# Kernel tuning notes

Hardware: AMD Instinct MI355X
Metric: run time of the kernel (lower is better)

## Reference

```python
import jax, jax.numpy as jnp
import numpy as np

N = 200_000   # nodes
E = 6_400_000 # edges (avg degree 32)


def setup_inputs() -> dict:
    key = jax.random.key(0)
    k = jax.random.split(key, 6)
    x = jax.random.normal(k[0], (N, 2), dtype=jnp.float32)
    edge_index = jax.random.randint(k[1], (2, E), 0, N, dtype=jnp.int32)
    # GCNConv(2, 8) and GCNConv(8, 4) parameters (Glorot-ish init, zero bias as in PyG)
    W1 = jax.random.normal(k[2], (2, 8), dtype=jnp.float32) * (1.0 / np.sqrt(2.0))
    b1 = jnp.zeros((8,), dtype=jnp.float32)
    W2 = jax.random.normal(k[3], (8, 4), dtype=jnp.float32) * (1.0 / np.sqrt(8.0))
    b2 = jnp.zeros((4,), dtype=jnp.float32)
    return {"x": x, "edge_index": edge_index, "W1": W1, "b1": b1, "W2": W2, "b2": b2}


def _gcn_conv(x, src, dst, norm, W, b, n):
    # PyG GCNConv: linear transform, normalized gather/scatter-add, bias after aggregation
    h = x @ W                                   # [N, F_out]
    msg = h[src] * norm[:, None]                # gather + edge-wise scale, [E', F_out]
    agg = jax.ops.segment_sum(msg, dst, num_segments=n)  # scatter-add at targets
    return agg + b


def reference(x, edge_index, W1, b1, W2, b2):
    n = x.shape[0]
    # add self-loops (PyG default add_self_loops=True)
    loops = jnp.arange(n, dtype=edge_index.dtype)
    src = jnp.concatenate([edge_index[0], loops])
    dst = jnp.concatenate([edge_index[1], loops])
    # symmetric degree normalization: deg computed at targets with unit edge weights
    deg = jax.ops.segment_sum(jnp.ones_like(src, dtype=x.dtype), dst, num_segments=n)
    deg_inv_sqrt = jnp.where(deg > 0, jax.lax.rsqrt(jnp.maximum(deg, 1.0)), 0.0)
    norm = deg_inv_sqrt[src] * deg_inv_sqrt[dst]  # [E']

    h = jax.nn.relu(_gcn_conv(x, src, dst, norm, W1, b1, n))
    out = _gcn_conv(h, src, dst, norm, W2, b2, n)
    return out
```

## Files before the change

### kernel.cpp

```cpp
#include <hip/hip_runtime.h>


#define EPB   8192
#define PART  2048
#define LPBIT 11
#define SRCB  18
#define BC    4
#define RSTR  2049
#define CAP   69632
#define STCAP 17408


__global__ __launch_bounds__(512) void sortA_kernel(
    const int* __restrict__ src, const int* __restrict__ dst,
    int* __restrict__ cursor, unsigned* __restrict__ packed, int E, int P) {
    __shared__ int cnt[128];
    int tid = threadIdx.x;
    if (tid < 128) cnt[tid] = 0;
    __syncthreads();
    int nv4 = E >> 2;
    int b4 = (blockIdx.x * EPB) >> 2;
    const int4* d4 = (const int4*)dst;
    const int4* s4 = (const int4*)src;
    int4 dv[4], sv[4];
    bool inb[4];
    #pragma unroll
    for (int k = 0; k < 4; k++) {
        int i = b4 + k * 512 + tid;
        inb[k] = (i < nv4);
        if (inb[k]) {
            dv[k] = d4[i];
            sv[k] = s4[i];
            atomicAdd(&cnt[dv[k].x >> LPBIT], 1);
            atomicAdd(&cnt[dv[k].y >> LPBIT], 1);
            atomicAdd(&cnt[dv[k].z >> LPBIT], 1);
            atomicAdd(&cnt[dv[k].w >> LPBIT], 1);
        }
    }
    bool lastblk = (blockIdx.x == gridDim.x - 1);
    int tsrc = 0, tdst = 0;
    bool tin = false;
    if (lastblk) {
        int e = (nv4 << 2) + tid;
        tin = (e < E);
        if (tin) {
            tdst = dst[e];
            tsrc = src[e];
            atomicAdd(&cnt[tdst >> LPBIT], 1);
        }
    }
    __syncthreads();
    if (tid < 128) {
        int c = cnt[tid];
        int base = (c > 0) ? atomicAdd(&cursor[tid], c) : 0;
        cnt[tid] = tid * CAP + base;
    }
    __syncthreads();
    #pragma unroll
    for (int k = 0; k < 4; k++) {
        if (inb[k]) {
            int4 d = dv[k];
            int4 s = sv[k];
            int p0 = atomicAdd(&cnt[d.x >> LPBIT], 1);
            packed[p0] = ((unsigned)(d.x & (PART - 1)) << SRCB) | (unsigned)s.x;
            int p1 = atomicAdd(&cnt[d.y >> LPBIT], 1);
            packed[p1] = ((unsigned)(d.y & (PART - 1)) << SRCB) | (unsigned)s.y;
            int p2 = atomicAdd(&cnt[d.z >> LPBIT], 1);
            packed[p2] = ((unsigned)(d.z & (PART - 1)) << SRCB) | (unsigned)s.z;
            int p3 = atomicAdd(&cnt[d.w >> LPBIT], 1);
            packed[p3] = ((unsigned)(d.w & (PART - 1)) << SRCB) | (unsigned)s.w;
        }
    }
    if (tin) {
        int pos = atomicAdd(&cnt[tdst >> LPBIT], 1);
        packed[pos] = ((unsigned)(tdst & (PART - 1)) << SRCB) | (unsigned)tsrc;
    }
}


__global__ __launch_bounds__(512) void localC_kernel(
    const unsigned* __restrict__ packed, const int* __restrict__ cursor,
    int* __restrict__ runStart, int* __restrict__ srcsorted) {
    __shared__ int hist[PART];
    __shared__ int sdata[512];
    __shared__ unsigned stage[STCAP];
    int tid = threadIdx.x;
    int dp = blockIdx.x >> 2, b = blockIdx.x & (BC - 1);
    int dpbase = dp * CAP;
    int tot = cursor[dp];
    int lo = dpbase + (int)(((long long)tot * b) / BC);
    int hi = dpbase + (int)(((long long)tot * (b + 1)) / BC);
    for (int k = tid; k < PART; k += 512) hist[k] = 0;
    __syncthreads();
    for (int i = lo + tid; i < hi; i += 512)
        atomicAdd(&hist[packed[i] >> SRCB], 1);
    __syncthreads();
    int off = tid * 4;
    int v0 = hist[off], v1 = hist[off + 1], v2 = hist[off + 2], v3 = hist[off + 3];
    int s = v0 + v1 + v2 + v3;
    int x = s;
    sdata[tid] = x;
    __syncthreads();
    for (int o = 1; o < 512; o <<= 1) {
        int t = (tid >= o) ? sdata[tid - o] : 0;
        __syncthreads();
        x += t;
        sdata[tid] = x;
        __syncthreads();
    }
    int run = x - s;
    int* rs = runStart + (size_t)(dp * BC + b) * RSTR;
    int c0 = lo + run, c1 = c0 + v0, c2 = c1 + v1, c3 = c2 + v2;
    rs[off] = c0; rs[off + 1] = c1; rs[off + 2] = c2; rs[off + 3] = c3;
    __syncthreads();
    hist[off] = c0; hist[off + 1] = c1; hist[off + 2] = c2; hist[off + 3] = c3;
    if (tid == 0) rs[PART] = hi;
    __syncthreads();
    int total = hi - lo;
    bool ovf = total > STCAP;
    for (int i = lo + tid; i < hi; i += 512) {
        unsigned w = packed[i];
        int pos = atomicAdd(&hist[w >> SRCB], 1);
        unsigned sv = w & ((1u << SRCB) - 1);
        if (!ovf) stage[pos - lo] = sv;
        else srcsorted[pos] = sv;
    }
    __syncthreads();
    if (!ovf)
        for (int j = tid; j < total; j += 512) srcsorted[lo + j] = (int)stage[j];
}


__global__ __launch_bounds__(512) void dinvg_kernel(
    const int* __restrict__ runStart, const float* __restrict__ x,
    float* __restrict__ dinv, float* __restrict__ g, int n) {
    int i = blockIdx.x * 512 + threadIdx.x;
    if (i >= n) return;
    int dp = i >> LPBIT, ld = i & (PART - 1);
    int deg = 0;
    #pragma unroll
    for (int b = 0; b < BC; b++) {
        const int* rs = runStart + (size_t)(dp * BC + b) * RSTR + ld;
        deg += rs[1] - rs[0];
    }
    float d = rsqrtf((float)deg + 1.0f);
    dinv[i] = d;
    float2 xv = ((const float2*)x)[i];
    ((float2*)g)[i] = make_float2(xv.x * d, xv.y * d);
}

__global__ __launch_bounds__(512) void agg1_kernel(
    const int* __restrict__ runStart, const int* __restrict__ srcsorted,
    const float* __restrict__ g, const float* __restrict__ dinv,
    const float* __restrict__ W1, const float* __restrict__ b1,
    const float* __restrict__ W2, float* __restrict__ hs2, int n) {
    int i = blockIdx.x * 512 + threadIdx.x;
    if (i >= n) return;
    int dp = i >> LPBIT, ld = i & (PART - 1);
    const float2* gp = (const float2*)g;
    float s0 = 0.0f, s1 = 0.0f;
    #pragma unroll
    for (int b = 0; b < BC; b++) {
        const int* rs = runStart + (size_t)(dp * BC + b) * RSTR + ld;
        int p0 = rs[0], p1 = rs[1];
        int p = p0;
        for (; p + 4 <= p1; p += 4) {
            int a = srcsorted[p], bb = srcsorted[p + 1];
            int c = srcsorted[p + 2], e = srcsorted[p + 3];
            float2 w0 = gp[a], w1 = gp[bb], w2 = gp[c], w3 = gp[e];
            s0 += w0.x + w1.x + w2.x + w3.x;
            s1 += w0.y + w1.y + w2.y + w3.y;
        }
        for (; p < p1; p++) {
            float2 w = gp[srcsorted[p]];
            s0 += w.x;
            s1 += w.y;
        }
    }
    float d = dinv[i];
    float2 gi = gp[i];
    s0 = (s0 + gi.x) * d;
    s1 = (s1 + gi.y) * d;
    float h[8];
    #pragma unroll
    for (int f = 0; f < 8; f++)
        h[f] = fmaxf(s0 * W1[f] + s1 * W1[8 + f] + b1[f], 0.0f);
    float oc[4];
    #pragma unroll
    for (int k = 0; k < 4; k++) {
        float a = 0.0f;
        #pragma unroll
        for (int f = 0; f < 8; f++) a += h[f] * W2[4 * f + k];
        oc[k] = a * d;
    }
    float4 o;
    o.x = oc[0]; o.y = oc[1]; o.z = oc[2]; o.w = oc[3];
    *(float4*)(hs2 + 4 * (size_t)i) = o;
}

__global__ __launch_bounds__(512) void agg2_kernel(
    const int* __restrict__ runStart, const int* __restrict__ srcsorted,
    const float* __restrict__ hs2, const float* __restrict__ dinv,
    const float* __restrict__ b2, float* __restrict__ out, int n) {
    int i = blockIdx.x * 512 + threadIdx.x;
    if (i >= n) return;
    int dp = i >> LPBIT, ld = i & (PART - 1);
    const float4* hp = (const float4*)hs2;
    float s0 = 0.0f, s1 = 0.0f, s2 = 0.0f, s3 = 0.0f;
    #pragma unroll
    for (int b = 0; b < BC; b++) {
        const int* rs = runStart + (size_t)(dp * BC + b) * RSTR + ld;
        int p0 = rs[0], p1 = rs[1];
        int p = p0;
        for (; p + 4 <= p1; p += 4) {
            int a = srcsorted[p], bb = srcsorted[p + 1];
            int c = srcsorted[p + 2], e = srcsorted[p + 3];
            float4 w0 = hp[a], w1 = hp[bb], w2 = hp[c], w3 = hp[e];
            s0 += w0.x + w1.x + w2.x + w3.x;
            s1 += w0.y + w1.y + w2.y + w3.y;
            s2 += w0.z + w1.z + w2.z + w3.z;
            s3 += w0.w + w1.w + w2.w + w3.w;
        }
        for (; p < p1; p++) {
            float4 w = hp[srcsorted[p]];
            s0 += w.x; s1 += w.y; s2 += w.z; s3 += w.w;
        }
    }
    float d = dinv[i];
    float4 hi2 = hp[i];
    float4 o;
    o.x = d * (s0 + hi2.x) + b2[0];
    o.y = d * (s1 + hi2.y) + b2[1];
    o.z = d * (s2 + hi2.z) + b2[2];
    o.w = d * (s3 + hi2.w) + b2[3];
    *(float4*)(out + 4 * (size_t)i) = o;
}

extern "C" void kernel_launch(void* const* d_in, const int* in_sizes, int n_in,
                              void* d_out, int out_size, void* d_ws, size_t ws_size,
                              hipStream_t stream) {
    const float* x   = (const float*)d_in[0];
    const int*   ei  = (const int*)d_in[1];
    const float* W1  = (const float*)d_in[2];
    const float* b1  = (const float*)d_in[3];
    const float* W2  = (const float*)d_in[4];
    const float* b2  = (const float*)d_in[5];
    float* out = (float*)d_out;

    const int n = in_sizes[0] / 2;
    const int E = in_sizes[1] / 2;
    const int* src = ei;
    const int* dst = ei + E;

    const int P  = (n + PART - 1) >> LPBIT;
    const int B1 = (E + EPB - 1) / EPB;

    int* ws = (int*)d_ws;
    int* cursor = ws;
    int* runStart = ws + 128;
    size_t rssz = (((size_t)P * BC * RSTR) + 3) & ~(size_t)3;
    unsigned* packed = (unsigned*)(runStart + rssz);
    int* srcsorted = (int*)(packed + (size_t)P * CAP);
    size_t nd = (size_t)P << LPBIT;
    float* dinv = (float*)packed;
    float* g    = dinv + nd;
    float* hs2  = g + 2 * nd;

    hipMemsetAsync(cursor, 0, 128 * sizeof(int), stream);

    const int gN = (n + 511) / 512;

    sortA_kernel <<<B1, 512, 0, stream>>>(src, dst, cursor, packed, E, P);
    localC_kernel<<<P * BC, 512, 0, stream>>>(packed, cursor, runStart, srcsorted);
    dinvg_kernel <<<gN, 512, 0, stream>>>(runStart, x, dinv, g, n);
    agg1_kernel  <<<gN, 512, 0, stream>>>(runStart, srcsorted, g, dinv, W1, b1, W2, hs2, n);
    agg2_kernel  <<<gN, 512, 0, stream>>>(runStart, srcsorted, hs2, dinv, b2, out, n);
}
```

Measured before the change: 247.6 us.

## Double sub-partitions, sort CSR in place, pad cursors, store start/end pairs

Halves edges per sort block and doubles the number of local sort blocks per destination partition, so more blocks run concurrently with a smaller shared staging buffer. The packed buffer is now overwritten in place with sorted sources, which drops the separate srcsorted array and its footprint. Run boundaries become int2 start/end pairs so each aggregation loads both bounds in one read. Global cursors are spaced 16 ints apart to avoid atomic contention on shared cache lines. In exchange the aggregation kernels walk eight runs per node instead of four, and the overflow fallback is gone, so a sub-partition larger than STCAP would overflow shared memory.

Result: slower. 258.7 us (+4.5%).

```diff
diff --git a/kernel.cpp b/kernel.cpp
--- a/kernel.cpp
+++ b/kernel.cpp
@@ -1,14 +1,14 @@
 #include <hip/hip_runtime.h>
 
 
-#define EPB   8192
+#define EPB   4096
 #define PART  2048
 #define LPBIT 11
 #define SRCB  18
-#define BC    4
-#define RSTR  2049
+#define BC    8
 #define CAP   69632
-#define STCAP 17408
+#define STCAP 8704
+#define CURSTR 16
 
 
 __global__ __launch_bounds__(512) void sortA_kernel(
@@ -19,13 +19,13 @@
     if (tid < 128) cnt[tid] = 0;
     __syncthreads();
     int nv4 = E >> 2;
-    int b4 = (blockIdx.x * EPB) >> 2;
+    int b4 = blockIdx.x * (EPB >> 2);
     const int4* d4 = (const int4*)dst;
     const int4* s4 = (const int4*)src;
-    int4 dv[4], sv[4];
-    bool inb[4];
-    #pragma unroll
-    for (int k = 0; k < 4; k++) {
+    int4 dv[2], sv[2];
+    bool inb[2];
+    #pragma unroll
+    for (int k = 0; k < 2; k++) {
         int i = b4 + k * 512 + tid;
         inb[k] = (i < nv4);
         if (inb[k]) {
@@ -52,12 +52,12 @@
     __syncthreads();
     if (tid < 128) {
         int c = cnt[tid];
-        int base = (c > 0) ? atomicAdd(&cursor[tid], c) : 0;
+        int base = (c > 0) ? atomicAdd(&cursor[tid * CURSTR], c) : 0;
         cnt[tid] = tid * CAP + base;
     }
     __syncthreads();
     #pragma unroll
-    for (int k = 0; k < 4; k++) {
+    for (int k = 0; k < 2; k++) {
         if (inb[k]) {
             int4 d = dv[k];
             int4 s = sv[k];
@@ -79,21 +79,21 @@
 
 
 __global__ __launch_bounds__(512) void localC_kernel(
-    const unsigned* __restrict__ packed, const int* __restrict__ cursor,
-    int* __restrict__ runStart, int* __restrict__ srcsorted) {
+    unsigned* __restrict__ csr,
+    const int* __restrict__ cursor, int* __restrict__ runSE) {
     __shared__ int hist[PART];
     __shared__ int sdata[512];
     __shared__ unsigned stage[STCAP];
     int tid = threadIdx.x;
-    int dp = blockIdx.x >> 2, b = blockIdx.x & (BC - 1);
+    int dp = blockIdx.x >> 3, b = blockIdx.x & (BC - 1);
     int dpbase = dp * CAP;
-    int tot = cursor[dp];
+    int tot = cursor[dp * CURSTR];
     int lo = dpbase + (int)(((long long)tot * b) / BC);
     int hi = dpbase + (int)(((long long)tot * (b + 1)) / BC);
     for (int k = tid; k < PART; k += 512) hist[k] = 0;
     __syncthreads();
     for (int i = lo + tid; i < hi; i += 512)
-        atomicAdd(&hist[packed[i] >> SRCB], 1);
+        atomicAdd(&hist[csr[i] >> SRCB], 1);
     __syncthreads();
     int off = tid * 4;
     int v0 = hist[off], v1 = hist[off + 1], v2 = hist[off + 2], v3 = hist[off + 3];
@@ -109,30 +109,28 @@
         __syncthreads();
     }
     int run = x - s;
-    int* rs = runStart + (size_t)(dp * BC + b) * RSTR;
     int c0 = lo + run, c1 = c0 + v0, c2 = c1 + v1, c3 = c2 + v2;
-    rs[off] = c0; rs[off + 1] = c1; rs[off + 2] = c2; rs[off + 3] = c3;
+    int2* se = (int2*)(runSE + (size_t)(dp * BC + b) * (2 * PART));
+    se[off]     = make_int2(c0, c1);
+    se[off + 1] = make_int2(c1, c2);
+    se[off + 2] = make_int2(c2, c3);
+    se[off + 3] = make_int2(c3, c3 + v3);
     __syncthreads();
     hist[off] = c0; hist[off + 1] = c1; hist[off + 2] = c2; hist[off + 3] = c3;
-    if (tid == 0) rs[PART] = hi;
     __syncthreads();
     int total = hi - lo;
-    bool ovf = total > STCAP;
     for (int i = lo + tid; i < hi; i += 512) {
-        unsigned w = packed[i];
+        unsigned w = csr[i];
         int pos = atomicAdd(&hist[w >> SRCB], 1);
-        unsigned sv = w & ((1u << SRCB) - 1);
-        if (!ovf) stage[pos - lo] = sv;
-        else srcsorted[pos] = sv;
-    }
-    __syncthreads();
-    if (!ovf)
-        for (int j = tid; j < total; j += 512) srcsorted[lo + j] = (int)stage[j];
+        stage[pos - lo] = w & ((1u << SRCB) - 1);
+    }
+    __syncthreads();
+    for (int j = tid; j < total; j += 512) csr[lo + j] = stage[j];
 }
 
 
 __global__ __launch_bounds__(512) void dinvg_kernel(
-    const int* __restrict__ runStart, const float* __restrict__ x,
+    const int* __restrict__ runSE, const float* __restrict__ x,
     float* __restrict__ dinv, float* __restrict__ g, int n) {
     int i = blockIdx.x * 512 + threadIdx.x;
     if (i >= n) return;
@@ -140,8 +138,8 @@
     int deg = 0;
     #pragma unroll
     for (int b = 0; b < BC; b++) {
-        const int* rs = runStart + (size_t)(dp * BC + b) * RSTR + ld;
-        deg += rs[1] - rs[0];
+        int2 se = ((const int2*)(runSE + (size_t)(dp * BC + b) * (2 * PART)))[ld];
+        deg += se.y - se.x;
     }
     float d = rsqrtf((float)deg + 1.0f);
     dinv[i] = d;
@@ -150,7 +148,7 @@
 }
 
 __global__ __launch_bounds__(512) void agg1_kernel(
-    const int* __restrict__ runStart, const int* __restrict__ srcsorted,
+    const int* __restrict__ runSE, const unsigned* __restrict__ csr,
     const float* __restrict__ g, const float* __restrict__ dinv,
     const float* __restrict__ W1, const float* __restrict__ b1,
     const float* __restrict__ W2, float* __restrict__ hs2, int n) {
@@ -161,18 +159,16 @@
     float s0 = 0.0f, s1 = 0.0f;
     #pragma unroll
     for (int b = 0; b < BC; b++) {
-        const int* rs = runStart + (size_t)(dp * BC + b) * RSTR + ld;
-        int p0 = rs[0], p1 = rs[1];
-        int p = p0;
+        int2 se = ((const int2*)(runSE + (size_t)(dp * BC + b) * (2 * PART)))[ld];
+        int p = se.x, p1 = se.y;
         for (; p + 4 <= p1; p += 4) {
-            int a = srcsorted[p], bb = srcsorted[p + 1];
-            int c = srcsorted[p + 2], e = srcsorted[p + 3];
+            int a = csr[p], bb = csr[p + 1], c = csr[p + 2], e = csr[p + 3];
             float2 w0 = gp[a], w1 = gp[bb], w2 = gp[c], w3 = gp[e];
             s0 += w0.x + w1.x + w2.x + w3.x;
             s1 += w0.y + w1.y + w2.y + w3.y;
         }
         for (; p < p1; p++) {
-            float2 w = gp[srcsorted[p]];
+            float2 w = gp[csr[p]];
             s0 += w.x;
             s1 += w.y;
         }
@@ -199,7 +195,7 @@
 }
 
 __global__ __launch_bounds__(512) void agg2_kernel(
-    const int* __restrict__ runStart, const int* __restrict__ srcsorted,
+    const int* __restrict__ runSE, const unsigned* __restrict__ csr,
     const float* __restrict__ hs2, const float* __restrict__ dinv,
     const float* __restrict__ b2, float* __restrict__ out, int n) {
     int i = blockIdx.x * 512 + threadIdx.x;
@@ -209,12 +205,10 @@
     float s0 = 0.0f, s1 = 0.0f, s2 = 0.0f, s3 = 0.0f;
     #pragma unroll
     for (int b = 0; b < BC; b++) {
-        const int* rs = runStart + (size_t)(dp * BC + b) * RSTR + ld;
-        int p0 = rs[0], p1 = rs[1];
-        int p = p0;
+        int2 se = ((const int2*)(runSE + (size_t)(dp * BC + b) * (2 * PART)))[ld];
+        int p = se.x, p1 = se.y;
         for (; p + 4 <= p1; p += 4) {
-            int a = srcsorted[p], bb = srcsorted[p + 1];
-            int c = srcsorted[p + 2], e = srcsorted[p + 3];
+            int a = csr[p], bb = csr[p + 1], c = csr[p + 2], e = csr[p + 3];
             float4 w0 = hp[a], w1 = hp[bb], w2 = hp[c], w3 = hp[e];
             s0 += w0.x + w1.x + w2.x + w3.x;
             s1 += w0.y + w1.y + w2.y + w3.y;
@@ -222,7 +216,7 @@
             s3 += w0.w + w1.w + w2.w + w3.w;
         }
         for (; p < p1; p++) {
-            float4 w = hp[srcsorted[p]];
+            float4 w = hp[csr[p]];
             s0 += w.x; s1 += w.y; s2 += w.z; s3 += w.w;
         }
     }
@@ -257,22 +251,21 @@
 
     int* ws = (int*)d_ws;
     int* cursor = ws;
-    int* runStart = ws + 128;
-    size_t rssz = (((size_t)P * BC * RSTR) + 3) & ~(size_t)3;
-    unsigned* packed = (unsigned*)(runStart + rssz);
-    int* srcsorted = (int*)(packed + (size_t)P * CAP);
+    int* runSE = ws + 128 * CURSTR;
+    size_t sesz = (size_t)P * BC * 2 * PART;
+    unsigned* csr = (unsigned*)(runSE + sesz);
     size_t nd = (size_t)P << LPBIT;
-    float* dinv = (float*)packed;
+    float* dinv = (float*)(csr + (size_t)P * CAP);
     float* g    = dinv + nd;
     float* hs2  = g + 2 * nd;
 
-    hipMemsetAsync(cursor, 0, 128 * sizeof(int), stream);
+    hipMemsetAsync(cursor, 0, 128 * CURSTR * sizeof(int), stream);
 
     const int gN = (n + 511) / 512;
 
-    sortA_kernel <<<B1, 512, 0, stream>>>(src, dst, cursor, packed, E, P);
-    localC_kernel<<<P * BC, 512, 0, stream>>>(packed, cursor, runStart, srcsorted);
-    dinvg_kernel <<<gN, 512, 0, stream>>>(runStart, x, dinv, g, n);
-    agg1_kernel  <<<gN, 512, 0, stream>>>(runStart, srcsorted, g, dinv, W1, b1, W2, hs2, n);
-    agg2_kernel  <<<gN, 512, 0, stream>>>(runStart, srcsorted, hs2, dinv, b2, out, n);
-}
+    sortA_kernel <<<B1, 512, 0, stream>>>(src, dst, cursor, csr, E, P);
+    localC_kernel<<<P * BC, 512, 0, stream>>>(csr, cursor, runSE);
+    dinvg_kernel <<<gN, 512, 0, stream>>>(runSE, x, dinv, g, n);
+    agg1_kernel  <<<gN, 512, 0, stream>>>(runSE, csr, g, dinv, W1, b1, W2, hs2, n);
+    agg2_kernel  <<<gN, 512, 0, stream>>>(runSE, csr, hs2, dinv, b2, out, n);
+}
```
